# Optimization experiments

Hardware: AMD Instinct MI355X
Metric: run time of the kernel (lower is better)

The kernel has to match this reference:

```python
import jax, jax.numpy as jnp
import numpy as np

N_NODES = 50000


def _mean_aggregate(x, src, dst):
    # gather source features along edges, segment-mean into destinations
    msg = x[src]                                             # [E, d] irregular gather
    agg = jax.ops.segment_sum(msg, dst, num_segments=N_NODES)  # [N, d]
    deg = jax.ops.segment_sum(jnp.ones((src.shape[0],), x.dtype), dst,
                              num_segments=N_NODES)
    return agg / jnp.maximum(deg, 1.0)[:, None]


def setup_inputs() -> dict:
    key = jax.random.key(0)
    ks = jax.random.split(key, 8)
    d_in, d_hid, d_out, L, E = 128, 128, 40, 3, 800000
    s = 1.0 / np.sqrt(d_hid)
    return {
        "x": jax.random.normal(ks[0], (N_NODES, d_in), jnp.float32),
        "edge_index": jax.random.randint(ks[1], (2, E), 0, N_NODES, jnp.int64),
        "Wl": jax.random.normal(ks[2], (L, d_hid, d_hid), jnp.float32) * s,
        "Wr": jax.random.normal(ks[3], (L, d_hid, d_hid), jnp.float32) * s,
        "bl": jnp.zeros((L, d_hid), jnp.float32),
        "W1": jax.random.normal(ks[4], (L * d_hid, d_hid), jnp.float32) * s,
        "b1": jnp.zeros((d_hid,), jnp.float32),
        "W2": jax.random.normal(ks[5], (d_hid, d_out), jnp.float32) * s,
        "b2": jnp.zeros((d_out,), jnp.float32),
    }


def reference(x, edge_index, Wl, Wr, bl, W1, b1, W2, b2):
    src, dst = edge_index[0], edge_index[1]
    h = x
    outs = []
    for i in range(Wl.shape[0]):  # num_layers (structurally small loop)
        m = _mean_aggregate(h, src, dst)          # mean_j x_j  [N, d]
        h = m @ Wl[i] + bl[i] + h @ Wr[i]         # SAGEConv: lin_l(aggr) + lin_r(x)
        outs.append(h)
    z = jnp.concatenate(outs, axis=1)             # [N, L*d]
    z = jax.nn.relu(z @ W1 + b1)
    z = z @ W2 + b2
    return jax.nn.log_softmax(z, axis=1)
```

## Files before the change

### kernel.cpp

```cpp
#include <hip/hip_runtime.h>
#include <math.h>

#define N_NODES 50000
#define D 128
#define LAYERS 3
#define DZ 384
#define DOUT 40
#define BUCKETS 196
#define BR 32

typedef __attribute__((ext_vector_type(4))) float f32x4;
typedef __attribute__((ext_vector_type(8))) short short8;

static __device__ __forceinline__ unsigned short f2bf(float f) {
    unsigned int u = __float_as_uint(f);
    u += 0x7FFFu + ((u >> 16) & 1u);
    return (unsigned short)(u >> 16);
}
static __device__ __forceinline__ float bf2f(unsigned short s) {
    return __uint_as_float(((unsigned int)s) << 16);
}


__global__ __launch_bounds__(256) void hist1_kernel(const int* __restrict__ dst, int E, int CH,
                                                    int nblk1, int* __restrict__ H) {
    __shared__ int h[BUCKETS];
    int t = threadIdx.x;
    if (t < BUCKETS) h[t] = 0;
    __syncthreads();
    int s = blockIdx.x * CH, e = min(E, s + CH);
    for (int i = s + t; i < e; i += 256) atomicAdd(&h[dst[i] >> 8], 1);
    __syncthreads();
    if (t < BUCKETS) H[t * nblk1 + blockIdx.x] = h[t];
}

__global__ __launch_bounds__(512) void scanS_kernel(int* __restrict__ H, int nblk1,
                                                    int* __restrict__ T) {
    __shared__ int s[512];
    int t = threadIdx.x, k = blockIdx.x;
    int v = (t < nblk1) ? H[k * nblk1 + t] : 0;
    s[t] = v;
    __syncthreads();
    for (int off = 1; off < 512; off <<= 1) {
        int u = (t >= off) ? s[t - off] : 0;
        __syncthreads();
        s[t] += u;
        __syncthreads();
    }
    if (t < nblk1) H[k * nblk1 + t] = s[t] - v;
    if (t == 511) T[k] = s[511];
}

__global__ __launch_bounds__(256) void bstart_kernel(const int* __restrict__ T,
                                                     int* __restrict__ bucketStart,
                                                     int* __restrict__ offs, int E) {
    __shared__ int s[256];
    int t = threadIdx.x;
    int v = (t < BUCKETS) ? T[t] : 0;
    s[t] = v;
    __syncthreads();
    for (int off = 1; off < 256; off <<= 1) {
        int u = (t >= off) ? s[t - off] : 0;
        __syncthreads();
        s[t] += u;
        __syncthreads();
    }
    if (t < BUCKETS) bucketStart[t] = s[t] - v;
    if (t == 0) { bucketStart[BUCKETS] = E; offs[N_NODES] = E; }
}

__global__ __launch_bounds__(256) void scatter_kernel(const int* __restrict__ src,
                                                      const int* __restrict__ dst, int E, int CH,
                                                      int nblk1, const int* __restrict__ H,
                                                      const int* __restrict__ bucketStart,
                                                      unsigned int* __restrict__ recs) {
    __shared__ int cur[BUCKETS];
    int t = threadIdx.x;
    if (t < BUCKETS) cur[t] = bucketStart[t] + H[t * nblk1 + blockIdx.x];
    __syncthreads();
    int s = blockIdx.x * CH, e = min(E, s + CH);
    for (int i = s + t; i < e; i += 256) {
        int d = dst[i];
        int pos = atomicAdd(&cur[d >> 8], 1);
        recs[pos] = (unsigned int)(src[i] & 0xFFFF) | ((unsigned int)(d & 255) << 16);
    }
}

__global__ __launch_bounds__(256) void bucket_csr_kernel(const unsigned int* __restrict__ recs,
                                                         const int* __restrict__ bucketStart,
                                                         int* __restrict__ offs,
                                                         unsigned short* __restrict__ adj) {
    __shared__ int h[256];
    __shared__ int sc[256];
    __shared__ int cur[256];
    int t = threadIdx.x, k = blockIdx.x;
    int bs = bucketStart[k], be = bucketStart[k + 1];
    h[t] = 0;
    __syncthreads();
    for (int i = bs + t; i < be; i += 256) atomicAdd(&h[(recs[i] >> 16) & 255], 1);
    __syncthreads();
    int v = h[t];
    sc[t] = v;
    __syncthreads();
    for (int off = 1; off < 256; off <<= 1) {
        int u = (t >= off) ? sc[t - off] : 0;
        __syncthreads();
        sc[t] += u;
        __syncthreads();
    }
    int excl = sc[t] - v;
    int node = k * 256 + t;
    if (node < N_NODES) offs[node] = bs + excl;
    cur[t] = bs + excl;
    __syncthreads();
    for (int i = bs + t; i < be; i += 256) {
        unsigned int r = recs[i];
        int pos = atomicAdd(&cur[(r >> 16) & 255], 1);
        adj[pos] = (unsigned short)(r & 0xFFFF);
    }
}

__global__ __launch_bounds__(256) void prep_kernel(const float* __restrict__ x,
                                                   const float* __restrict__ Wl,
                                                   const float* __restrict__ Wr,
                                                   const float* __restrict__ W1,
                                                   const float* __restrict__ W2,
                                                   unsigned short* __restrict__ xb,
                                                   unsigned short* __restrict__ WT,
                                                   unsigned short* __restrict__ W1T,
                                                   unsigned short* __restrict__ W2T,
                                                   int n4) {
    int i = blockIdx.x * blockDim.x + threadIdx.x;
    if (i < n4) {
        const float4 v = ((const float4*)x)[i];
        unsigned int lo = ((unsigned int)f2bf(v.y) << 16) | f2bf(v.x);
        unsigned int hi = ((unsigned int)f2bf(v.w) << 16) | f2bf(v.z);
        ((unsigned int*)xb)[i * 2] = lo;
        ((unsigned int*)xb)[i * 2 + 1] = hi;
        return;
    }
    int j = i - n4;
    if (j < LAYERS * 128 * 256) {
        int layer = j >> 15;
        int r = j & 32767;
        int c = r >> 8, k = r & 255;
        const float* W = (k < 128) ? (Wl + layer * 16384) : (Wr + layer * 16384);
        WT[j] = f2bf(W[(k & 127) * 128 + c]);
        return;
    }
    j -= LAYERS * 128 * 256;
    if (j < 128 * 384) {
        int c = j / 384, k = j - c * 384;
        W1T[j] = f2bf(W1[k * 128 + c]);
        return;
    }
    j -= 128 * 384;
    if (j < 48 * 128) {
        int c = j >> 7, k = j & 127;
        W2T[j] = (c < DOUT) ? f2bf(W2[k * DOUT + c]) : (unsigned short)0;
    }
}

__global__ __launch_bounds__(256) void sage_fused_kernel(
        const unsigned short* __restrict__ h, int ldh,
        const int* __restrict__ offs, const unsigned short* __restrict__ adj,
        const unsigned short* __restrict__ WT,
        const float* __restrict__ bl,
        unsigned short* __restrict__ zout, int ldz) {
    __shared__ unsigned short mlds[BR][136];
    int tid = threadIdx.x;
    int wid = tid >> 6;
    int lane = tid & 63;
    int grp = lane >> 4, l16 = lane & 15;
    int r0 = blockIdx.x * BR;

    for (int i = 0; i < 8; ++i) {
        int nn = wid * 8 + i;
        int node = r0 + nn;
        float acc[8];
#pragma unroll
        for (int j = 0; j < 8; ++j) acc[j] = 0.f;
        int s = 0, e = 0;
        if (node < N_NODES) { s = offs[node]; e = offs[node + 1]; }
        int k = s + grp;
        for (; k + 4 < e; k += 8) {
            int s0 = adj[k], s1 = adj[k + 4];
            short8 v0 = *(const short8*)(h + (size_t)s0 * ldh + l16 * 8);
            short8 v1 = *(const short8*)(h + (size_t)s1 * ldh + l16 * 8);
#pragma unroll
            for (int j = 0; j < 8; ++j)
                acc[j] += bf2f((unsigned short)v0[j]) + bf2f((unsigned short)v1[j]);
        }
        if (k < e) {
            int s0 = adj[k];
            short8 v0 = *(const short8*)(h + (size_t)s0 * ldh + l16 * 8);
#pragma unroll
            for (int j = 0; j < 8; ++j) acc[j] += bf2f((unsigned short)v0[j]);
        }
#pragma unroll
        for (int j = 0; j < 8; ++j) {
            float a = acc[j];
            a += __shfl_xor(a, 16);
            a += __shfl_xor(a, 32);
            acc[j] = a;
        }
        if (grp == 0) {
            float inv = 1.f / fmaxf((float)(e - s), 1.f);
            uint4 o;
            o.x = ((unsigned int)f2bf(acc[1] * inv) << 16) | f2bf(acc[0] * inv);
            o.y = ((unsigned int)f2bf(acc[3] * inv) << 16) | f2bf(acc[2] * inv);
            o.z = ((unsigned int)f2bf(acc[5] * inv) << 16) | f2bf(acc[4] * inv);
            o.w = ((unsigned int)f2bf(acc[7] * inv) << 16) | f2bf(acc[6] * inv);
            *(uint4*)(&mlds[nn][l16 * 8]) = o;
        }
    }
    __syncthreads();

    int lrow = lane & 15;
    int lk8 = (lane >> 4) * 8;
    f32x4 acc0[2], acc1[2];
#pragma unroll
    for (int t = 0; t < 2; ++t) { acc0[t] = (f32x4){0.f,0.f,0.f,0.f}; acc1[t] = (f32x4){0.f,0.f,0.f,0.f}; }

    int rA = r0 + lrow, rB = r0 + 16 + lrow;
    int rAc = (rA < N_NODES) ? rA : (N_NODES - 1);
    int rBc = (rB < N_NODES) ? rB : (N_NODES - 1);
    const unsigned short* aH0 = h + (size_t)rAc * ldh + lk8;
    const unsigned short* aH1 = h + (size_t)rBc * ldh + lk8;
    int colBase = wid * 32;

#pragma unroll
    for (int kc = 0; kc < 8; ++kc) {
        short8 aF0, aF1;
        if (kc < 4) {
            aF0 = *(const short8*)(&mlds[lrow][kc * 32 + lk8]);
            aF1 = *(const short8*)(&mlds[16 + lrow][kc * 32 + lk8]);
        } else {
            aF0 = *(const short8*)(aH0 + (kc - 4) * 32);
            aF1 = *(const short8*)(aH1 + (kc - 4) * 32);
        }
#pragma unroll
        for (int ctl = 0; ctl < 2; ++ctl) {
            short8 bF = *(const short8*)(WT + (size_t)(colBase + ctl * 16 + lrow) * 256 + kc * 32 + lk8);
            acc0[ctl] = __builtin_amdgcn_mfma_f32_16x16x32_bf16(aF0, bF, acc0[ctl], 0, 0, 0);
            acc1[ctl] = __builtin_amdgcn_mfma_f32_16x16x32_bf16(aF1, bF, acc1[ctl], 0, 0, 0);
        }
    }

    int ocol = lane & 15;
    int orow0 = r0 + (lane >> 4) * 4;
#pragma unroll
    for (int ctl = 0; ctl < 2; ++ctl) {
        int col = colBase + ctl * 16 + ocol;
        float b = bl[col];
#pragma unroll
        for (int j = 0; j < 4; ++j) {
            int ra = orow0 + j;
            int rb = ra + 16;
            if (ra < N_NODES) zout[(size_t)ra * ldz + col] = f2bf(acc0[ctl][j] + b);
            if (rb < N_NODES) zout[(size_t)rb * ldz + col] = f2bf(acc1[ctl][j] + b);
        }
    }
}

__global__ __launch_bounds__(256) void mlp_fused_kernel(
        const unsigned short* __restrict__ zB,
        const unsigned short* __restrict__ W1T,
        const float* __restrict__ b1,
        const unsigned short* __restrict__ W2T,
        const float* __restrict__ b2,
        float* __restrict__ out) {
    __shared__ unsigned short z1lds[BR][136];
    int tid = threadIdx.x;
    int wid = tid >> 6;
    int lane = tid & 63;
    int r0 = blockIdx.x * BR;
    int lrow = lane & 15;
    int lk8 = (lane >> 4) * 8;

    f32x4 acc0[2], acc1[2];
#pragma unroll
    for (int t = 0; t < 2; ++t) { acc0[t] = (f32x4){0.f,0.f,0.f,0.f}; acc1[t] = (f32x4){0.f,0.f,0.f,0.f}; }

    int rA = r0 + lrow, rB = r0 + 16 + lrow;
    int rAc = (rA < N_NODES) ? rA : (N_NODES - 1);
    int rBc = (rB < N_NODES) ? rB : (N_NODES - 1);
    const unsigned short* aP0 = zB + (size_t)rAc * DZ + lk8;
    const unsigned short* aP1 = zB + (size_t)rBc * DZ + lk8;
    int colBase = wid * 32;

#pragma unroll
    for (int kc = 0; kc < 12; ++kc) {
        short8 aF0 = *(const short8*)(aP0 + kc * 32);
        short8 aF1 = *(const short8*)(aP1 + kc * 32);
#pragma unroll
        for (int ctl = 0; ctl < 2; ++ctl) {
            short8 bF = *(const short8*)(W1T + (size_t)(colBase + ctl * 16 + lrow) * DZ + kc * 32 + lk8);
            acc0[ctl] = __builtin_amdgcn_mfma_f32_16x16x32_bf16(aF0, bF, acc0[ctl], 0, 0, 0);
            acc1[ctl] = __builtin_amdgcn_mfma_f32_16x16x32_bf16(aF1, bF, acc1[ctl], 0, 0, 0);
        }
    }

    int ocol = lane & 15;
    int lrow0 = (lane >> 4) * 4;
#pragma unroll
    for (int ctl = 0; ctl < 2; ++ctl) {
        int col = colBase + ctl * 16 + ocol;
        float b = b1[col];
#pragma unroll
        for (int j = 0; j < 4; ++j) {
            z1lds[lrow0 + j][col] = f2bf(fmaxf(acc0[ctl][j] + b, 0.f));
            z1lds[16 + lrow0 + j][col] = f2bf(fmaxf(acc1[ctl][j] + b, 0.f));
        }
    }
    __syncthreads();

    if (wid < 2) {
        f32x4 acc[3];
#pragma unroll
        for (int t = 0; t < 3; ++t) acc[t] = (f32x4){0.f,0.f,0.f,0.f};
        int lr = wid * 16 + lrow;
#pragma unroll
        for (int kc = 0; kc < 4; ++kc) {
            short8 aF = *(const short8*)(&z1lds[lr][kc * 32 + lk8]);
#pragma unroll
            for (int ct = 0; ct < 3; ++ct) {
                short8 bF = *(const short8*)(W2T + (size_t)(ct * 16 + lrow) * 128 + kc * 32 + lk8);
                acc[ct] = __builtin_amdgcn_mfma_f32_16x16x32_bf16(aF, bF, acc[ct], 0, 0, 0);
            }
        }

        float b0 = b2[ocol];
        float b1v = b2[16 + ocol];
        float b2v = (ocol < 8) ? b2[32 + ocol] : 0.f;

#pragma unroll
        for (int j = 0; j < 4; ++j) {
            int orow = r0 + wid * 16 + (lane >> 4) * 4 + j;
            float v0 = acc[0][j] + b0;
            float v1 = acc[1][j] + b1v;
            float v2 = (ocol < 8) ? (acc[2][j] + b2v) : -1e30f;
            float mx = fmaxf(fmaxf(v0, v1), v2);
            mx = fmaxf(mx, __shfl_xor(mx, 1));
            mx = fmaxf(mx, __shfl_xor(mx, 2));
            mx = fmaxf(mx, __shfl_xor(mx, 4));
            mx = fmaxf(mx, __shfl_xor(mx, 8));
            float es = expf(v0 - mx) + expf(v1 - mx) + ((ocol < 8) ? expf(v2 - mx) : 0.f);
            es += __shfl_xor(es, 1);
            es += __shfl_xor(es, 2);
            es += __shfl_xor(es, 4);
            es += __shfl_xor(es, 8);
            float ls = logf(es);
            if (orow < N_NODES) {
                out[(size_t)orow * DOUT + ocol] = v0 - mx - ls;
                out[(size_t)orow * DOUT + 16 + ocol] = v1 - mx - ls;
                if (ocol < 8) out[(size_t)orow * DOUT + 32 + ocol] = v2 - mx - ls;
            }
        }
    }
}


extern "C" void kernel_launch(void* const* d_in, const int* in_sizes, int n_in,
                              void* d_out, int out_size, void* d_ws, size_t ws_size,
                              hipStream_t stream) {
    const float* x   = (const float*)d_in[0];
    const int*   ei  = (const int*)d_in[1];
    const float* Wl  = (const float*)d_in[2];
    const float* Wr  = (const float*)d_in[3];
    const float* bl  = (const float*)d_in[4];
    const float* W1  = (const float*)d_in[5];
    const float* b1  = (const float*)d_in[6];
    const float* W2  = (const float*)d_in[7];
    const float* b2  = (const float*)d_in[8];
    float* out = (float*)d_out;

    const int E = in_sizes[1] / 2;
    const int* src = ei;
    const int* dst = ei + E;

    int CH = 2048;
    int nblk1 = (E + CH - 1) / CH;
    if (nblk1 > 512) { CH = ((E + 511) / 512 + 255) & ~255; nblk1 = (E + CH - 1) / CH; }

    char* p = (char*)d_ws;
    auto take = [&p](size_t bytes) { char* q = p; p += (bytes + 255) & ~(size_t)255; return q; };
    int* offs        = (int*)take((N_NODES + 1) * sizeof(int));
    int* H           = (int*)take((size_t)BUCKETS * nblk1 * sizeof(int));
    int* T           = (int*)take(BUCKETS * sizeof(int));
    int* bucketStart = (int*)take((BUCKETS + 1) * sizeof(int));
    unsigned int*   recs = (unsigned int*)take((size_t)E * sizeof(unsigned int));
    unsigned short* adj  = (unsigned short*)take((size_t)E * sizeof(unsigned short));
    unsigned short* xb  = (unsigned short*)take((size_t)N_NODES * D * 2);
    unsigned short* z   = (unsigned short*)take((size_t)N_NODES * DZ * 2);
    unsigned short* WT  = (unsigned short*)take((size_t)LAYERS * 128 * 256 * 2);
    unsigned short* W1T = (unsigned short*)take((size_t)128 * 384 * 2);
    unsigned short* W2T = (unsigned short*)take((size_t)48 * 128 * 2);

    int n4 = N_NODES * D / 4;
    int prep_total = n4 + LAYERS * 128 * 256 + 128 * 384 + 48 * 128;
    prep_kernel<<<(prep_total + 255) / 256, 256, 0, stream>>>(
        x, Wl, Wr, W1, W2, xb, WT, W1T, W2T, n4);

    hist1_kernel<<<nblk1, 256, 0, stream>>>(dst, E, CH, nblk1, H);
    scanS_kernel<<<BUCKETS, 512, 0, stream>>>(H, nblk1, T);
    bstart_kernel<<<1, 256, 0, stream>>>(T, bucketStart, offs, E);
    scatter_kernel<<<nblk1, 256, 0, stream>>>(src, dst, E, CH, nblk1, H, bucketStart, recs);
    bucket_csr_kernel<<<BUCKETS, 256, 0, stream>>>(recs, bucketStart, offs, adj);

    int fgrid = (N_NODES + BR - 1) / BR;

    for (int i = 0; i < LAYERS; ++i) {
        const unsigned short* hin = (i == 0) ? xb : (z + (size_t)(i - 1) * D);
        int ldh = (i == 0) ? D : DZ;
        sage_fused_kernel<<<fgrid, 256, 0, stream>>>(
            hin, ldh, offs, adj, WT + (size_t)i * 128 * 256, bl + (size_t)i * D,
            z + (size_t)i * D, DZ);
    }

    mlp_fused_kernel<<<fgrid, 256, 0, stream>>>(z, W1T, b1, W2T, b2, out);
}
```

Baseline: 235.0 us.

## Split layer outputs into contiguous buffers and remap gather to one node per half-wave

New measurement: 225.9 us. 1.04x faster.

```diff
diff --git a/kernel.cpp b/kernel.cpp
--- a/kernel.cpp
+++ b/kernel.cpp
@@ -17,8 +17,21 @@
     u += 0x7FFFu + ((u >> 16) & 1u);
     return (unsigned short)(u >> 16);
 }
-static __device__ __forceinline__ float bf2f(unsigned short s) {
-    return __uint_as_float(((unsigned int)s) << 16);
+static __device__ __forceinline__ float bflo(unsigned int u) {
+    return __uint_as_float(u << 16);
+}
+static __device__ __forceinline__ float bfhi(unsigned int u) {
+    return __uint_as_float(u & 0xFFFF0000u);
+}
+static __device__ __forceinline__ void accq(float* acc, uint4 q, float wgt) {
+    acc[0] = fmaf(wgt, bflo(q.x), acc[0]);
+    acc[1] = fmaf(wgt, bfhi(q.x), acc[1]);
+    acc[2] = fmaf(wgt, bflo(q.y), acc[2]);
+    acc[3] = fmaf(wgt, bfhi(q.y), acc[3]);
+    acc[4] = fmaf(wgt, bflo(q.z), acc[4]);
+    acc[5] = fmaf(wgt, bfhi(q.z), acc[5]);
+    acc[6] = fmaf(wgt, bflo(q.w), acc[6]);
+    acc[7] = fmaf(wgt, bfhi(q.w), acc[7]);
 }
 
 
@@ -119,6 +132,7 @@
         adj[pos] = (unsigned short)(r & 0xFFFF);
     }
 }
+
 
 __global__ __launch_bounds__(256) void prep_kernel(const float* __restrict__ x,
                                                    const float* __restrict__ Wl,
@@ -162,60 +176,56 @@
 }
 
 __global__ __launch_bounds__(256) void sage_fused_kernel(
-        const unsigned short* __restrict__ h, int ldh,
+        const unsigned short* __restrict__ h,
         const int* __restrict__ offs, const unsigned short* __restrict__ adj,
         const unsigned short* __restrict__ WT,
         const float* __restrict__ bl,
-        unsigned short* __restrict__ zout, int ldz) {
+        unsigned short* __restrict__ zout) {
     __shared__ unsigned short mlds[BR][136];
     int tid = threadIdx.x;
-    int wid = tid >> 6;
-    int lane = tid & 63;
-    int grp = lane >> 4, l16 = lane & 15;
     int r0 = blockIdx.x * BR;
-
-    for (int i = 0; i < 8; ++i) {
-        int nn = wid * 8 + i;
+    int gid = tid >> 4, l16 = tid & 15;
+
+    const unsigned short* hb = h + l16 * 8;
+#pragma unroll
+    for (int t = 0; t < 2; ++t) {
+        int nn = gid * 2 + t;
         int node = r0 + nn;
         float acc[8];
 #pragma unroll
         for (int j = 0; j < 8; ++j) acc[j] = 0.f;
         int s = 0, e = 0;
         if (node < N_NODES) { s = offs[node]; e = offs[node + 1]; }
-        int k = s + grp;
-        for (; k + 4 < e; k += 8) {
-            int s0 = adj[k], s1 = adj[k + 4];
-            short8 v0 = *(const short8*)(h + (size_t)s0 * ldh + l16 * 8);
-            short8 v1 = *(const short8*)(h + (size_t)s1 * ldh + l16 * 8);
-#pragma unroll
-            for (int j = 0; j < 8; ++j)
-                acc[j] += bf2f((unsigned short)v0[j]) + bf2f((unsigned short)v1[j]);
-        }
-        if (k < e) {
-            int s0 = adj[k];
-            short8 v0 = *(const short8*)(h + (size_t)s0 * ldh + l16 * 8);
-#pragma unroll
-            for (int j = 0; j < 8; ++j) acc[j] += bf2f((unsigned short)v0[j]);
-        }
-#pragma unroll
-        for (int j = 0; j < 8; ++j) {
-            float a = acc[j];
-            a += __shfl_xor(a, 16);
-            a += __shfl_xor(a, 32);
-            acc[j] = a;
-        }
-        if (grp == 0) {
-            float inv = 1.f / fmaxf((float)(e - s), 1.f);
-            uint4 o;
-            o.x = ((unsigned int)f2bf(acc[1] * inv) << 16) | f2bf(acc[0] * inv);
-            o.y = ((unsigned int)f2bf(acc[3] * inv) << 16) | f2bf(acc[2] * inv);
-            o.z = ((unsigned int)f2bf(acc[5] * inv) << 16) | f2bf(acc[4] * inv);
-            o.w = ((unsigned int)f2bf(acc[7] * inv) << 16) | f2bf(acc[6] * inv);
-            *(uint4*)(&mlds[nn][l16 * 8]) = o;
-        }
-    }
-    __syncthreads();
-
+        for (int k = s; k < e; k += 4) {
+            int e1 = e - 1;
+            int a0 = adj[k];
+            int a1 = adj[min(k + 1, e1)];
+            int a2 = adj[min(k + 2, e1)];
+            int a3 = adj[min(k + 3, e1)];
+            uint4 q0 = *(const uint4*)(hb + (size_t)a0 * D);
+            uint4 q1 = *(const uint4*)(hb + (size_t)a1 * D);
+            uint4 q2 = *(const uint4*)(hb + (size_t)a2 * D);
+            uint4 q3 = *(const uint4*)(hb + (size_t)a3 * D);
+            float w1 = (k + 1 < e) ? 1.f : 0.f;
+            float w2 = (k + 2 < e) ? 1.f : 0.f;
+            float w3 = (k + 3 < e) ? 1.f : 0.f;
+            accq(acc, q0, 1.f);
+            accq(acc, q1, w1);
+            accq(acc, q2, w2);
+            accq(acc, q3, w3);
+        }
+        float inv = 1.f / fmaxf((float)(e - s), 1.f);
+        uint4 o;
+        o.x = ((unsigned int)f2bf(acc[1] * inv) << 16) | f2bf(acc[0] * inv);
+        o.y = ((unsigned int)f2bf(acc[3] * inv) << 16) | f2bf(acc[2] * inv);
+        o.z = ((unsigned int)f2bf(acc[5] * inv) << 16) | f2bf(acc[4] * inv);
+        o.w = ((unsigned int)f2bf(acc[7] * inv) << 16) | f2bf(acc[6] * inv);
+        *(uint4*)(&mlds[nn][l16 * 8]) = o;
+    }
+    __syncthreads();
+
+    int wid = tid >> 6;
+    int lane = tid & 63;
     int lrow = lane & 15;
     int lk8 = (lane >> 4) * 8;
     f32x4 acc0[2], acc1[2];
@@ -225,8 +235,8 @@
     int rA = r0 + lrow, rB = r0 + 16 + lrow;
     int rAc = (rA < N_NODES) ? rA : (N_NODES - 1);
     int rBc = (rB < N_NODES) ? rB : (N_NODES - 1);
-    const unsigned short* aH0 = h + (size_t)rAc * ldh + lk8;
-    const unsigned short* aH1 = h + (size_t)rBc * ldh + lk8;
+    const unsigned short* aH0 = h + (size_t)rAc * D + lk8;
+    const unsigned short* aH1 = h + (size_t)rBc * D + lk8;
     int colBase = wid * 32;
 
 #pragma unroll
@@ -257,14 +267,16 @@
         for (int j = 0; j < 4; ++j) {
             int ra = orow0 + j;
             int rb = ra + 16;
-            if (ra < N_NODES) zout[(size_t)ra * ldz + col] = f2bf(acc0[ctl][j] + b);
-            if (rb < N_NODES) zout[(size_t)rb * ldz + col] = f2bf(acc1[ctl][j] + b);
+            if (ra < N_NODES) zout[(size_t)ra * D + col] = f2bf(acc0[ctl][j] + b);
+            if (rb < N_NODES) zout[(size_t)rb * D + col] = f2bf(acc1[ctl][j] + b);
         }
     }
 }
 
 __global__ __launch_bounds__(256) void mlp_fused_kernel(
-        const unsigned short* __restrict__ zB,
+        const unsigned short* __restrict__ z0,
+        const unsigned short* __restrict__ z1b,
+        const unsigned short* __restrict__ z2,
         const unsigned short* __restrict__ W1T,
         const float* __restrict__ b1,
         const unsigned short* __restrict__ W2T,
@@ -285,14 +297,14 @@
     int rA = r0 + lrow, rB = r0 + 16 + lrow;
     int rAc = (rA < N_NODES) ? rA : (N_NODES - 1);
     int rBc = (rB < N_NODES) ? rB : (N_NODES - 1);
-    const unsigned short* aP0 = zB + (size_t)rAc * DZ + lk8;
-    const unsigned short* aP1 = zB + (size_t)rBc * DZ + lk8;
+    const unsigned short* zb[3] = {z0, z1b, z2};
     int colBase = wid * 32;
 
 #pragma unroll
     for (int kc = 0; kc < 12; ++kc) {
-        short8 aF0 = *(const short8*)(aP0 + kc * 32);
-        short8 aF1 = *(const short8*)(aP1 + kc * 32);
+        const unsigned short* base = zb[kc >> 2];
+        short8 aF0 = *(const short8*)(base + (size_t)rAc * D + (kc & 3) * 32 + lk8);
+        short8 aF1 = *(const short8*)(base + (size_t)rBc * D + (kc & 3) * 32 + lk8);
 #pragma unroll
         for (int ctl = 0; ctl < 2; ++ctl) {
             short8 bF = *(const short8*)(W1T + (size_t)(colBase + ctl * 16 + lrow) * DZ + kc * 32 + lk8);
@@ -392,7 +404,9 @@
     unsigned int*   recs = (unsigned int*)take((size_t)E * sizeof(unsigned int));
     unsigned short* adj  = (unsigned short*)take((size_t)E * sizeof(unsigned short));
     unsigned short* xb  = (unsigned short*)take((size_t)N_NODES * D * 2);
-    unsigned short* z   = (unsigned short*)take((size_t)N_NODES * DZ * 2);
+    unsigned short* z0  = (unsigned short*)take((size_t)N_NODES * D * 2);
+    unsigned short* z1  = (unsigned short*)take((size_t)N_NODES * D * 2);
+    unsigned short* z2  = (unsigned short*)take((size_t)N_NODES * D * 2);
     unsigned short* WT  = (unsigned short*)take((size_t)LAYERS * 128 * 256 * 2);
     unsigned short* W1T = (unsigned short*)take((size_t)128 * 384 * 2);
     unsigned short* W2T = (unsigned short*)take((size_t)48 * 128 * 2);
@@ -410,13 +424,12 @@
 
     int fgrid = (N_NODES + BR - 1) / BR;
 
+    unsigned short* zs[3] = {z0, z1, z2};
     for (int i = 0; i < LAYERS; ++i) {
-        const unsigned short* hin = (i == 0) ? xb : (z + (size_t)(i - 1) * D);
-        int ldh = (i == 0) ? D : DZ;
+        const unsigned short* hin = (i == 0) ? xb : zs[i - 1];
         sage_fused_kernel<<<fgrid, 256, 0, stream>>>(
-            hin, ldh, offs, adj, WT + (size_t)i * 128 * 256, bl + (size_t)i * D,
-            z + (size_t)i * D, DZ);
-    }
-
-    mlp_fused_kernel<<<fgrid, 256, 0, stream>>>(z, W1T, b1, W2T, b2, out);
-}
+            hin, offs, adj, WT + (size_t)i * 128 * 256, bl + (size_t)i * D, zs[i]);
+    }
+
+    mlp_fused_kernel<<<fgrid, 256, 0, stream>>>(z0, z1, z2, W1T, b1, W2T, b2, out);
+}
```
